# Kernel tuning notes

Measured on AMD Instinct MI355X. Metric: run time of the kernel, lower is better.

## Reference

```python
import jax, jax.numpy as jnp
import numpy as np

DIMS = 1024
STATE = 2 * DIMS
EPS = 1e-8


def _rmsnorm(v, scale):
    # norm = ||v||_2 * d^{-1/2}
    d = v.shape[-1]
    n = jnp.sqrt(jnp.sum(v * v, axis=-1, keepdims=True)) * (d ** -0.5)
    return scale * v / (n + EPS)


def setup_inputs() -> dict:
    key = jax.random.key(0)
    ks = jax.random.split(key, 5)
    x = jax.random.normal(ks[0], (4, 2048, DIMS), dtype=jnp.float32)
    ls_scale = jnp.ones((DIMS // 2,), dtype=jnp.float32)
    rs_scale = jnp.ones((DIMS // 2,), dtype=jnp.float32)
    split_scale = jnp.full((DIMS,), 0.1, dtype=jnp.float32)
    sk = (1.0 / DIMS) ** 0.5
    Wk = jax.random.uniform(ks[1], (DIMS, STATE), jnp.float32, -sk, sk)
    Wugg = jax.random.uniform(ks[2], (DIMS, 3 * STATE), jnp.float32, -sk, sk)
    so = (1.0 / STATE) ** 0.5
    Wout = jax.random.uniform(ks[3], (STATE, DIMS), jnp.float32, -so, so)
    return {"x": x, "ls_scale": ls_scale, "rs_scale": rs_scale,
            "split_scale": split_scale, "Wk": Wk, "Wugg": Wugg, "Wout": Wout}


def reference(x, ls_scale, rs_scale, split_scale, Wk, Wugg, Wout):
    residual = x
    # RMS_split norm (output_dim=None)
    xl, xr = jnp.split(x, 2, axis=-1)
    xn = jnp.concatenate([_rmsnorm(xl, ls_scale), _rmsnorm(xr, rs_scale)], axis=-1)
    xn = xn * split_scale

    K = jax.nn.sigmoid(xn @ Wk)                      # [B,S,STATE]
    u, g_in, g_out = jnp.split(xn @ Wugg, 3, axis=-1)
    u = u * jax.nn.sigmoid(g_in) * (1.0 - K)

    # linear recurrence: h_0 = u_0; h_t = K_{t-1} * h_{t-1} + u_t
    a = jnp.concatenate([jnp.ones_like(K[..., :1, :]), K[..., :-1, :]], axis=-2)

    def combine(lhs, rhs):
        aL, bL = lhs
        aR, bR = rhs
        return (aL * aR, bL * aR + bR)

    _, h = jax.lax.associative_scan(combine, (a, u), axis=1)
    outputs = h * jax.nn.sigmoid(g_out)
    y = outputs @ Wout
    return y + residual
```

## Files before the change

kernel.cpp:

```cpp
#include <hip/hip_runtime.h>
#include <hip/hip_bf16.h>
#include <hip/hip_fp8.h>
#include <stdint.h>

#define DIMS 1024
#define STATE 2048
#define BATCH 4
#define SEQ 2048
#define TOKENS 8192
#define N1 8192
#define NCHUNK 16
#define CHUNKL (SEQ / NCHUNK)

typedef __hip_bfloat16 bf16;
typedef unsigned char u8;
typedef unsigned short u16;
typedef __attribute__((ext_vector_type(4))) float f32x4;
typedef __attribute__((ext_vector_type(16))) float f32x16;
typedef __attribute__((ext_vector_type(2))) long v2i64;

#define XN_SCALE 32.0f
#define W1_SCALE 256.0f
#define H_SCALE  32.0f
#define W2_SCALE 256.0f
#define INV_SCALE (1.0f / 8192.0f)

__device__ __forceinline__ float sigmoidf_(float x) {
  return 1.0f / (1.0f + __expf(-x));
}

__device__ __forceinline__ u8 to_fp8(float f) {
  __hip_fp8_e4m3 h(f);
  return h.__x;
}

__device__ __forceinline__ float b2f(u16 v) {
  union { uint32_t u; float f; } w;
  w.u = ((uint32_t)v) << 16;
  return w.f;
}

__device__ __forceinline__ u16 f2b(float f) {
  bf16 h = __float2bfloat16(f);
  return *(u16*)&h;
}

__device__ __forceinline__ int kperm(int k) {
  return (k & ~24) | ((k & 8) << 1) | ((k & 16) >> 1);
}

__device__ __forceinline__ void async_copy16(const void* g, void* l) {
  __builtin_amdgcn_global_load_lds(
      (const __attribute__((address_space(1))) void*)(uintptr_t)g,
      (__attribute__((address_space(3))) void*)(uint32_t)(uintptr_t)l,
      16, 0, 0);
}

__device__ __forceinline__ int swz32(int row, int kc) {
  int line = row >> 1;
  int sub = ((row & 1) << 2) | kc;
  return (line << 3) | (sub ^ (line & 7));
}
__device__ __forceinline__ void swz32_dec(int c, int& row, int& kc) {
  int line = c >> 3;
  int sub = (c & 7) ^ (line & 7);
  row = (line << 1) | (sub >> 2);
  kc = sub & 3;
}

__device__ __forceinline__ int xcd_swz(int wg, int nwg) {
  return (wg & 7) * (nwg >> 3) + (wg >> 3);
}

__global__ __launch_bounds__(256) void transpose_fp8_kernel(
    const float* __restrict__ W, u8* __restrict__ Wt, int K, int N,
    int stream_base, int interleave, float scale) {
  __shared__ float tile[32][33];
  int tx = threadIdx.x & 31;
  int ty = threadIdx.x >> 5;
  long col = (long)blockIdx.x * 32 + tx;
  long rowb = (long)blockIdx.y * 32;
#pragma unroll
  for (int i = 0; i < 32; i += 8)
    tile[ty + i][tx] = W[(rowb + ty + i) * N + col];
  __syncthreads();
  long ocol = rowb + kperm(tx);
  long orow = (long)blockIdx.x * 32 + ty;
#pragma unroll
  for (int i = 0; i < 32; i += 8) {
    long n = orow + i;
    long dstrow = interleave ? (((n & 2047) << 2) | (stream_base + (n >> 11))) : n;
    Wt[dstrow * K + ocol] = to_fp8(tile[tx][ty + i] * scale);
  }
}

__global__ __launch_bounds__(256) void rmsnorm_kernel(
    const float* __restrict__ x, const float* __restrict__ ls,
    const float* __restrict__ rs, const float* __restrict__ ss,
    u8* __restrict__ xn8) {
  int token = blockIdx.x;
  int tid = threadIdx.x;
  const float4* xt = (const float4*)(x + (long)token * DIMS);
  float4 v = xt[tid];
  float s = v.x * v.x + v.y * v.y + v.z * v.z + v.w * v.w;
#pragma unroll
  for (int d = 32; d > 0; d >>= 1) s += __shfl_down(s, d);
  __shared__ float parts[4];
  if ((tid & 63) == 0) parts[tid >> 6] = s;
  __syncthreads();
  int j = tid * 4;
  bool left = j < 512;
  float sum = left ? (parts[0] + parts[1]) : (parts[2] + parts[3]);
  float n = sqrtf(sum * (1.0f / 512.0f));
  float inv = 1.0f / (n + 1e-8f);
  const float4* sc = (const float4*)(left ? ls : rs);
  float4 g = sc[left ? tid : tid - 128];
  float4 p = ((const float4*)ss)[tid];
  u8 q[4];
  q[0] = to_fp8(v.x * g.x * inv * p.x * XN_SCALE);
  q[1] = to_fp8(v.y * g.y * inv * p.y * XN_SCALE);
  q[2] = to_fp8(v.z * g.z * inv * p.z * XN_SCALE);
  q[3] = to_fp8(v.w * g.w * inv * p.w * XN_SCALE);
  *(uint32_t*)(xn8 + (long)token * DIMS + kperm(j)) = *(uint32_t*)q;
}

__device__ __forceinline__ void g1f8_stage(const u8* __restrict__ A,
                                           const u8* __restrict__ Bt,
                                           long arow0, long brow0, int k0,
                                           int wave, int lane, u8* As, u8* Bs) {
  const int K = DIMS;
#pragma unroll
  for (int i = 0; i < 4; i++) {
    int c = (wave * 4 + i) * 64 + lane;
    int row, kc; swz32_dec(c, row, kc);
    async_copy16(A + (arow0 + row) * K + k0 + kc * 16, (char*)As + (wave * 4 + i) * 1024);
  }
#pragma unroll
  for (int i = 0; i < 2; i++) {
    int c = (wave * 2 + i) * 64 + lane;
    int row, kc; swz32_dec(c, row, kc);
    async_copy16(Bt + (brow0 + row) * K + k0 + kc * 16, (char*)Bs + (wave * 2 + i) * 1024);
  }
}

__global__ __launch_bounds__(256, 2) void gemm1_fp8(
    const u8* __restrict__ A, const u8* __restrict__ Bt,
    uint32_t* __restrict__ AU, u16* __restrict__ GO) {
  __shared__ __align__(16) u8 As[3][256 * 64];
  __shared__ __align__(16) u8 Bs[3][128 * 64];
  int tid = threadIdx.x;
  int lane = tid & 63, wave = tid >> 6;
  int wm = wave & 1, wn = wave >> 1;
  int wg = xcd_swz(blockIdx.y * gridDim.x + blockIdx.x, gridDim.x * gridDim.y);
  int bx = wg & (gridDim.x - 1);
  int by = wg >> 6;
  long arow0 = (long)by * 256;
  long brow0 = (long)bx * 128;
  int m_lane = lane & 31, q4 = lane >> 5;
  f32x16 acc[4][2] = {};

  g1f8_stage(A, Bt, arow0, brow0, 0, wave, lane, As[0], Bs[0]);
  g1f8_stage(A, Bt, arow0, brow0, 64, wave, lane, As[1], Bs[1]);

  int cur = 0, nxt = 2;
  for (int it = 0; it < 16; ++it) {
    if (it == 15) asm volatile("s_waitcnt vmcnt(0)" ::: "memory");
    else          asm volatile("s_waitcnt vmcnt(6)" ::: "memory");
    __builtin_amdgcn_s_barrier();
    __builtin_amdgcn_sched_barrier(0);
    if (it + 2 < 16)
      g1f8_stage(A, Bt, arow0, brow0, (it + 2) * 64, wave, lane, As[nxt], Bs[nxt]);
    const u8* Asc = As[cur];
    const u8* Bsc = Bs[cur];
    v2i64 af[2][4], bfr[2][2];
#pragma unroll
    for (int p = 0; p < 2; p++) {
#pragma unroll
      for (int mt = 0; mt < 4; mt++)
        af[p][mt] = *(const v2i64*)(Asc + swz32(wm * 128 + mt * 32 + m_lane, p * 2 + q4) * 16);
#pragma unroll
      for (int nt = 0; nt < 2; nt++)
        bfr[p][nt] = *(const v2i64*)(Bsc + swz32(wn * 64 + nt * 32 + m_lane, p * 2 + q4) * 16);
    }
    __builtin_amdgcn_s_setprio(1);
#pragma unroll
    for (int p = 0; p < 2; p++)
#pragma unroll
      for (int mt = 0; mt < 4; mt++)
#pragma unroll
        for (int nt = 0; nt < 2; nt++) {
          acc[mt][nt] = __builtin_amdgcn_mfma_f32_32x32x16_fp8_fp8(bfr[p][nt][0], af[p][mt][0], acc[mt][nt], 0, 0, 0);
          acc[mt][nt] = __builtin_amdgcn_mfma_f32_32x32x16_fp8_fp8(bfr[p][nt][1], af[p][mt][1], acc[mt][nt], 0, 0, 0);
        }
    __builtin_amdgcn_s_setprio(0);
    cur = cur == 2 ? 0 : cur + 1;
    nxt = nxt == 2 ? 0 : nxt + 1;
  }

#pragma unroll
  for (int mt = 0; mt < 4; mt++) {
    long row = arow0 + wm * 128 + mt * 32 + m_lane;
    long rb = row * STATE;
#pragma unroll
    for (int nt = 0; nt < 2; nt++) {
#pragma unroll
      for (int g = 0; g < 4; g++) {
        long col = brow0 + wn * 64 + nt * 32 + g * 8 + q4 * 4;
        long ch = col >> 2;
        float kraw = acc[mt][nt][g * 4 + 0] * INV_SCALE;
        float uraw = acc[mt][nt][g * 4 + 1] * INV_SCALE;
        float gin  = acc[mt][nt][g * 4 + 2] * INV_SCALE;
        float gout = acc[mt][nt][g * 4 + 3] * INV_SCALE;
        float ah = sigmoidf_(kraw);
        float uu = uraw * sigmoidf_(gin) * (1.0f - ah);
        u16 pr[2];
        pr[0] = f2b(ah);
        pr[1] = f2b(uu);
        AU[rb + ch] = *(uint32_t*)pr;
        GO[rb + ch] = f2b(sigmoidf_(gout));
      }
    }
  }
}

__device__ __forceinline__ void g2f8_stage(const u8* __restrict__ A,
                                           const u8* __restrict__ Bt,
                                           long arow0, long brow0, int k0,
                                           int wave, int lane, u8* As, u8* Bs) {
  const int K = STATE;
#pragma unroll
  for (int i = 0; i < 2; i++) {
    int c = (wave * 2 + i) * 64 + lane;
    int row, kc; swz32_dec(c, row, kc);
    async_copy16(A + (arow0 + row) * K + k0 + kc * 16, (char*)As + (wave * 2 + i) * 1024);
  }
#pragma unroll
  for (int i = 0; i < 2; i++) {
    int c = (wave * 2 + i) * 64 + lane;
    int row, kc; swz32_dec(c, row, kc);
    async_copy16(Bt + (brow0 + row) * K + k0 + kc * 16, (char*)Bs + (wave * 2 + i) * 1024);
  }
}

__global__ __launch_bounds__(256) void gemm2_fp8(
    const u8* __restrict__ A, const u8* __restrict__ Bt,
    float* __restrict__ C, const float* __restrict__ resid) {
  __shared__ __align__(16) u8 As[3][128 * 64];
  __shared__ __align__(16) u8 Bs[3][128 * 64];
  int tid = threadIdx.x;
  int lane = tid & 63, wave = tid >> 6;
  int wm = wave & 1, wn = wave >> 1;
  int wg = xcd_swz(blockIdx.y * gridDim.x + blockIdx.x, gridDim.x * gridDim.y);
  int bx = wg & (gridDim.x - 1);
  int by = wg >> 3;
  long arow0 = (long)by * 128;
  long brow0 = (long)bx * 128;
  int m_lane = lane & 31, q4 = lane >> 5;
  f32x16 acc[2][2] = {};

  g2f8_stage(A, Bt, arow0, brow0, 0, wave, lane, As[0], Bs[0]);
  g2f8_stage(A, Bt, arow0, brow0, 64, wave, lane, As[1], Bs[1]);

  int cur = 0, nxt = 2;
  for (int it = 0; it < 32; ++it) {
    if (it == 31) asm volatile("s_waitcnt vmcnt(0)" ::: "memory");
    else          asm volatile("s_waitcnt vmcnt(4)" ::: "memory");
    __builtin_amdgcn_s_barrier();
    __builtin_amdgcn_sched_barrier(0);
    if (it + 2 < 32)
      g2f8_stage(A, Bt, arow0, brow0, (it + 2) * 64, wave, lane, As[nxt], Bs[nxt]);
    const u8* Asc = As[cur];
    const u8* Bsc = Bs[cur];
    v2i64 af[2][2], bfr[2][2];
#pragma unroll
    for (int p = 0; p < 2; p++) {
#pragma unroll
      for (int mt = 0; mt < 2; mt++)
        af[p][mt] = *(const v2i64*)(Asc + swz32(wm * 64 + mt * 32 + m_lane, p * 2 + q4) * 16);
#pragma unroll
      for (int nt = 0; nt < 2; nt++)
        bfr[p][nt] = *(const v2i64*)(Bsc + swz32(wn * 64 + nt * 32 + m_lane, p * 2 + q4) * 16);
    }
    __builtin_amdgcn_s_setprio(1);
#pragma unroll
    for (int p = 0; p < 2; p++)
#pragma unroll
      for (int mt = 0; mt < 2; mt++)
#pragma unroll
        for (int nt = 0; nt < 2; nt++) {
          acc[mt][nt] = __builtin_amdgcn_mfma_f32_32x32x16_fp8_fp8(bfr[p][nt][0], af[p][mt][0], acc[mt][nt], 0, 0, 0);
          acc[mt][nt] = __builtin_amdgcn_mfma_f32_32x32x16_fp8_fp8(bfr[p][nt][1], af[p][mt][1], acc[mt][nt], 0, 0, 0);
        }
    __builtin_amdgcn_s_setprio(0);
    cur = cur == 2 ? 0 : cur + 1;
    nxt = nxt == 2 ? 0 : nxt + 1;
  }
#pragma unroll
  for (int mt = 0; mt < 2; mt++) {
    long row = arow0 + wm * 64 + mt * 32 + m_lane;
#pragma unroll
    for (int nt = 0; nt < 2; nt++) {
#pragma unroll
      for (int g = 0; g < 4; g++) {
        long col = brow0 + wn * 64 + nt * 32 + g * 8 + q4 * 4;
        float4 rv = *(const float4*)(resid + row * DIMS + col);
        float4 ov;
        ov.x = acc[mt][nt][g * 4 + 0] * INV_SCALE + rv.x;
        ov.y = acc[mt][nt][g * 4 + 1] * INV_SCALE + rv.y;
        ov.z = acc[mt][nt][g * 4 + 2] * INV_SCALE + rv.z;
        ov.w = acc[mt][nt][g * 4 + 3] * INV_SCALE + rv.w;
        *(float4*)(C + row * DIMS + col) = ov;
      }
    }
  }
}

__global__ __launch_bounds__(256) void chunk_summary_kernel(
    const uint32_t* __restrict__ AU, float* __restrict__ carryA,
    float* __restrict__ carryU) {
  int b = blockIdx.x;
  int ch = blockIdx.y * 256 + threadIdx.x;
  int chunk = blockIdx.z;
  int t0 = chunk * CHUNKL;
  const uint32_t* base = AU + (long)b * SEQ * STATE + ch;
  float ap = 1.0f;
  if (chunk != 0) ap = b2f((u16)(base[(long)(t0 - 1) * STATE] & 0xffff));
  float A = 1.0f, U = 0.0f;
#pragma unroll 8
  for (int t = t0; t < t0 + CHUNKL; t++) {
    uint32_t w = base[(long)t * STATE];
    float ah = b2f((u16)(w & 0xffff));
    float u  = b2f((u16)(w >> 16));
    A *= ap;
    U = ap * U + u;
    ap = ah;
  }
  int cidx = (b * NCHUNK + chunk) * STATE + ch;
  carryA[cidx] = A;
  carryU[cidx] = U;
}

__global__ __launch_bounds__(256) void carry_scan_kernel(
    const float* __restrict__ carryA, const float* __restrict__ carryU,
    float* __restrict__ carryIn) {
  int idx = blockIdx.x * 256 + threadIdx.x;
  int b = idx >> 11;
  int ch = idx & 2047;
  float h = 0.0f;
#pragma unroll
  for (int c = 0; c < NCHUNK; c++) {
    int cidx = (b * NCHUNK + c) * STATE + ch;
    carryIn[cidx] = h;
    h = carryA[cidx] * h + carryU[cidx];
  }
}

__global__ __launch_bounds__(256) void scan_chunk_kernel(
    const uint32_t* __restrict__ AU, const u16* __restrict__ GO,
    const float* __restrict__ carryIn, u8* __restrict__ sco8) {
  int b = blockIdx.x;
  int c0 = blockIdx.y * 32;
  int chunk = blockIdx.z;
  int tstart = chunk * CHUNKL;
  __shared__ float a_s[32][65], u_s[32][65], h_s[32][65];
  int tid = threadIdx.x;
  int lane = tid & 63, wave = tid >> 6;
  int cc = tid & 31;
  int tq = tid >> 5;

  float carryH[8], carryK[8];
#pragma unroll
  for (int i = 0; i < 8; i++) {
    int ch = c0 + wave * 8 + i;
    carryH[i] = carryIn[(b * NCHUNK + chunk) * STATE + ch];
    carryK[i] = (chunk == 0)
                    ? 1.0f
                    : b2f((u16)(AU[((long)(b * SEQ + tstart - 1)) * STATE + ch] & 0xffff));
  }

  float g_r[8];
  for (int t0 = tstart; t0 < tstart + CHUNKL; t0 += 64) {
#pragma unroll
    for (int i = 0; i < 8; i++) {
      int t = tq * 8 + i;
      long idx = ((long)(b * SEQ + t0 + t)) * STATE + c0 + cc;
      uint32_t w = AU[idx];
      a_s[cc][t] = b2f((u16)(w & 0xffff));
      u_s[cc][t] = b2f((u16)(w >> 16));
      g_r[i] = b2f(GO[idx]);
    }
    __syncthreads();
#pragma unroll
    for (int i = 0; i < 8; i++) {
      int ch = wave * 8 + i;
      float aK = a_s[ch][lane];
      float u = u_s[ch][lane];
      float a = __shfl_up(aK, 1);
      if (lane == 0) a = carryK[i];
      float A = a, U = u;
#pragma unroll
      for (int d = 1; d < 64; d <<= 1) {
        float Au = __shfl_up(A, d);
        float Uu = __shfl_up(U, d);
        if (lane >= d) { U += A * Uu; A *= Au; }
      }
      float h = U + A * carryH[i];
      carryH[i] = __shfl(h, 63);
      carryK[i] = __shfl(aK, 63);
      h_s[ch][lane] = h;
    }
    __syncthreads();
#pragma unroll
    for (int i = 0; i < 8; i++) {
      int t = tq * 8 + i;
      sco8[((long)(b * SEQ + t0 + t)) * STATE + c0 + kperm(cc)] =
          to_fp8(h_s[cc][t] * g_r[i] * H_SCALE);
    }
    __syncthreads();
  }
}

extern "C" void kernel_launch(void* const* d_in, const int* in_sizes, int n_in,
                              void* d_out, int out_size, void* d_ws, size_t ws_size,
                              hipStream_t stream) {
  const float* x    = (const float*)d_in[0];
  const float* ls   = (const float*)d_in[1];
  const float* rs   = (const float*)d_in[2];
  const float* ss   = (const float*)d_in[3];
  const float* Wk   = (const float*)d_in[4];
  const float* Wugg = (const float*)d_in[5];
  const float* Wout = (const float*)d_in[6];
  float* out = (float*)d_out;

  char* ws = (char*)d_ws;
  u8*   W1f8 = (u8*)ws;
  u8*   W2f8 = (u8*)(ws + 8388608);
  u8*   xn8  = (u8*)(ws + 10485760);
  uint32_t* AU = (uint32_t*)(ws + 18874368);
  u16*  GOb  = (u16*)(ws + 18874368 + 67108864);
  u8*   sco8 = (u8*)(ws + 18874368 + 67108864 + 33554432);
  float* carryA  = (float*)xn8;
  float* carryU  = carryA + BATCH * NCHUNK * STATE;
  float* carryIn = carryU + BATCH * NCHUNK * STATE;

  transpose_fp8_kernel<<<dim3(STATE / 32, DIMS / 32), 256, 0, stream>>>(
      Wk, W1f8, DIMS, STATE, 0, 1, W1_SCALE);
  transpose_fp8_kernel<<<dim3(3 * STATE / 32, DIMS / 32), 256, 0, stream>>>(
      Wugg, W1f8, DIMS, 3 * STATE, 1, 1, W1_SCALE);
  transpose_fp8_kernel<<<dim3(DIMS / 32, STATE / 32), 256, 0, stream>>>(
      Wout, W2f8, STATE, DIMS, 0, 0, W2_SCALE);

  rmsnorm_kernel<<<TOKENS, 256, 0, stream>>>(x, ls, rs, ss, xn8);

  gemm1_fp8<<<dim3(N1 / 128, TOKENS / 256), 256, 0, stream>>>(xn8, W1f8, AU, GOb);

  chunk_summary_kernel<<<dim3(BATCH, STATE / 256, NCHUNK), 256, 0, stream>>>(
      AU, carryA, carryU);
  carry_scan_kernel<<<dim3(BATCH * STATE / 256), 256, 0, stream>>>(
      carryA, carryU, carryIn);
  scan_chunk_kernel<<<dim3(BATCH, STATE / 32, NCHUNK), 256, 0, stream>>>(
      AU, GOb, carryIn, sco8);

  gemm2_fp8<<<dim3(DIMS / 128, TOKENS / 128), 256, 0, stream>>>(
      sco8, W2f8, out, x);
}
```

Baseline: 399.6 us.

## Enlarge gemm1 tile to 256x256 with 8 waves and phased load/MFMA interleave

The first FP8 GEMM now uses 256x256 output tiles computed by 512 threads (8 waves, 2x4) instead of 256x128 tiles with 4 waves. Each K step is split into four phases, and each phase issues one slice of the next stage's async global-to-LDS copies alongside a small batch of MFMAs, separated by barriers. The aim is better operand reuse per byte loaded and finer overlap of memory traffic with matrix math. In exchange, LDS use rises to about 96KB per block, which likely limits the CU to one resident block, and each K step now has many more barriers.

```diff
diff --git a/kernel.cpp b/kernel.cpp
--- a/kernel.cpp
+++ b/kernel.cpp
@@ -124,77 +124,124 @@
   *(uint32_t*)(xn8 + (long)token * DIMS + kperm(j)) = *(uint32_t*)q;
 }
 
-__device__ __forceinline__ void g1f8_stage(const u8* __restrict__ A,
-                                           const u8* __restrict__ Bt,
-                                           long arow0, long brow0, int k0,
-                                           int wave, int lane, u8* As, u8* Bs) {
-  const int K = DIMS;
-#pragma unroll
-  for (int i = 0; i < 4; i++) {
-    int c = (wave * 4 + i) * 64 + lane;
+__device__ __forceinline__ void g1_stage_q(
+    const u8* __restrict__ A, const u8* __restrict__ Bt,
+    long arow0, long brow0, int k0, int q, int wave, int lane,
+    u8* As, u8* Bs) {
+  int cb = q * 512 + wave * 64;
+  int c = cb + lane;
+  if (cb < 1024) {
     int row, kc; swz32_dec(c, row, kc);
-    async_copy16(A + (arow0 + row) * K + k0 + kc * 16, (char*)As + (wave * 4 + i) * 1024);
-  }
-#pragma unroll
-  for (int i = 0; i < 2; i++) {
-    int c = (wave * 2 + i) * 64 + lane;
-    int row, kc; swz32_dec(c, row, kc);
-    async_copy16(Bt + (brow0 + row) * K + k0 + kc * 16, (char*)Bs + (wave * 2 + i) * 1024);
-  }
-}
-
-__global__ __launch_bounds__(256, 2) void gemm1_fp8(
+    async_copy16(A + (arow0 + row) * DIMS + k0 + kc * 16, As + cb * 16);
+  } else {
+    int row, kc; swz32_dec(c - 1024, row, kc);
+    async_copy16(Bt + (brow0 + row) * DIMS + k0 + kc * 16, Bs + (cb - 1024) * 16);
+  }
+}
+
+__global__ __launch_bounds__(512, 2) void gemm1_fp8(
     const u8* __restrict__ A, const u8* __restrict__ Bt,
     uint32_t* __restrict__ AU, u16* __restrict__ GO) {
   __shared__ __align__(16) u8 As[3][256 * 64];
-  __shared__ __align__(16) u8 Bs[3][128 * 64];
+  __shared__ __align__(16) u8 Bs[3][256 * 64];
   int tid = threadIdx.x;
-  int lane = tid & 63, wave = tid >> 6;
-  int wm = wave & 1, wn = wave >> 1;
+  int lane = tid & 63;
+  int wave = tid >> 6;
+  int wm = wave >> 2;
+  int wn = wave & 3;
   int wg = xcd_swz(blockIdx.y * gridDim.x + blockIdx.x, gridDim.x * gridDim.y);
-  int bx = wg & (gridDim.x - 1);
-  int by = wg >> 6;
+  int bx = wg & 31;
+  int by = wg >> 5;
   long arow0 = (long)by * 256;
-  long brow0 = (long)bx * 128;
+  long brow0 = (long)bx * 256;
   int m_lane = lane & 31, q4 = lane >> 5;
   f32x16 acc[4][2] = {};
 
-  g1f8_stage(A, Bt, arow0, brow0, 0, wave, lane, As[0], Bs[0]);
-  g1f8_stage(A, Bt, arow0, brow0, 64, wave, lane, As[1], Bs[1]);
-
-  int cur = 0, nxt = 2;
-  for (int it = 0; it < 16; ++it) {
-    if (it == 15) asm volatile("s_waitcnt vmcnt(0)" ::: "memory");
-    else          asm volatile("s_waitcnt vmcnt(6)" ::: "memory");
-    __builtin_amdgcn_s_barrier();
+#pragma unroll
+  for (int q = 0; q < 4; q++)
+    g1_stage_q(A, Bt, arow0, brow0, 0, q, wave, lane, As[0], Bs[0]);
+#pragma unroll
+  for (int q = 0; q < 4; q++)
+    g1_stage_q(A, Bt, arow0, brow0, 64, q, wave, lane, As[1], Bs[1]);
+  asm volatile("s_waitcnt vmcnt(4)" ::: "memory");
+  __builtin_amdgcn_s_barrier();
+
+  int bufc = 0, bufn = 2;
+  for (int t = 0; t < 16; ++t) {
+    const u8* Asc = As[bufc];
+    const u8* Bsc = Bs[bufc];
+    u8* Asn = As[bufn];
+    u8* Bsn = Bs[bufn];
+    int k2 = (t + 2) * 64;
+    bool pf = (t + 2 < 16);
+    v2i64 af[4], bfr;
+
+#pragma unroll
+    for (int mt = 0; mt < 4; mt++)
+      af[mt] = *(const v2i64*)(Asc + swz32(wm * 128 + mt * 32 + m_lane, q4) * 16);
+    bfr = *(const v2i64*)(Bsc + swz32(wn * 64 + m_lane, q4) * 16);
+    if (pf) g1_stage_q(A, Bt, arow0, brow0, k2, 0, wave, lane, Asn, Bsn);
+    __builtin_amdgcn_s_barrier();
+    asm volatile("s_waitcnt lgkmcnt(0)" ::: "memory");
     __builtin_amdgcn_sched_barrier(0);
-    if (it + 2 < 16)
-      g1f8_stage(A, Bt, arow0, brow0, (it + 2) * 64, wave, lane, As[nxt], Bs[nxt]);
-    const u8* Asc = As[cur];
-    const u8* Bsc = Bs[cur];
-    v2i64 af[2][4], bfr[2][2];
-#pragma unroll
-    for (int p = 0; p < 2; p++) {
-#pragma unroll
-      for (int mt = 0; mt < 4; mt++)
-        af[p][mt] = *(const v2i64*)(Asc + swz32(wm * 128 + mt * 32 + m_lane, p * 2 + q4) * 16);
-#pragma unroll
-      for (int nt = 0; nt < 2; nt++)
-        bfr[p][nt] = *(const v2i64*)(Bsc + swz32(wn * 64 + nt * 32 + m_lane, p * 2 + q4) * 16);
-    }
     __builtin_amdgcn_s_setprio(1);
 #pragma unroll
-    for (int p = 0; p < 2; p++)
-#pragma unroll
-      for (int mt = 0; mt < 4; mt++)
-#pragma unroll
-        for (int nt = 0; nt < 2; nt++) {
-          acc[mt][nt] = __builtin_amdgcn_mfma_f32_32x32x16_fp8_fp8(bfr[p][nt][0], af[p][mt][0], acc[mt][nt], 0, 0, 0);
-          acc[mt][nt] = __builtin_amdgcn_mfma_f32_32x32x16_fp8_fp8(bfr[p][nt][1], af[p][mt][1], acc[mt][nt], 0, 0, 0);
-        }
+    for (int mt = 0; mt < 4; mt++) {
+      acc[mt][0] = __builtin_amdgcn_mfma_f32_32x32x16_fp8_fp8(bfr[0], af[mt][0], acc[mt][0], 0, 0, 0);
+      acc[mt][0] = __builtin_amdgcn_mfma_f32_32x32x16_fp8_fp8(bfr[1], af[mt][1], acc[mt][0], 0, 0, 0);
+    }
     __builtin_amdgcn_s_setprio(0);
-    cur = cur == 2 ? 0 : cur + 1;
-    nxt = nxt == 2 ? 0 : nxt + 1;
+    __builtin_amdgcn_s_barrier();
+
+    bfr = *(const v2i64*)(Bsc + swz32(wn * 64 + 32 + m_lane, q4) * 16);
+    if (pf) g1_stage_q(A, Bt, arow0, brow0, k2, 1, wave, lane, Asn, Bsn);
+    __builtin_amdgcn_s_barrier();
+    asm volatile("s_waitcnt lgkmcnt(0)" ::: "memory");
+    __builtin_amdgcn_sched_barrier(0);
+    __builtin_amdgcn_s_setprio(1);
+#pragma unroll
+    for (int mt = 0; mt < 4; mt++) {
+      acc[mt][1] = __builtin_amdgcn_mfma_f32_32x32x16_fp8_fp8(bfr[0], af[mt][0], acc[mt][1], 0, 0, 0);
+      acc[mt][1] = __builtin_amdgcn_mfma_f32_32x32x16_fp8_fp8(bfr[1], af[mt][1], acc[mt][1], 0, 0, 0);
+    }
+    __builtin_amdgcn_s_setprio(0);
+    __builtin_amdgcn_s_barrier();
+
+#pragma unroll
+    for (int mt = 0; mt < 4; mt++)
+      af[mt] = *(const v2i64*)(Asc + swz32(wm * 128 + mt * 32 + m_lane, 2 + q4) * 16);
+    bfr = *(const v2i64*)(Bsc + swz32(wn * 64 + m_lane, 2 + q4) * 16);
+    if (pf) g1_stage_q(A, Bt, arow0, brow0, k2, 2, wave, lane, Asn, Bsn);
+    __builtin_amdgcn_s_barrier();
+    asm volatile("s_waitcnt lgkmcnt(0)" ::: "memory");
+    __builtin_amdgcn_sched_barrier(0);
+    __builtin_amdgcn_s_setprio(1);
+#pragma unroll
+    for (int mt = 0; mt < 4; mt++) {
+      acc[mt][0] = __builtin_amdgcn_mfma_f32_32x32x16_fp8_fp8(bfr[0], af[mt][0], acc[mt][0], 0, 0, 0);
+      acc[mt][0] = __builtin_amdgcn_mfma_f32_32x32x16_fp8_fp8(bfr[1], af[mt][1], acc[mt][0], 0, 0, 0);
+    }
+    __builtin_amdgcn_s_setprio(0);
+    __builtin_amdgcn_s_barrier();
+
+    bfr = *(const v2i64*)(Bsc + swz32(wn * 64 + 32 + m_lane, 2 + q4) * 16);
+    if (pf) g1_stage_q(A, Bt, arow0, brow0, k2, 3, wave, lane, Asn, Bsn);
+    if (pf) asm volatile("s_waitcnt vmcnt(4)" ::: "memory");
+    else    asm volatile("s_waitcnt vmcnt(0)" ::: "memory");
+    __builtin_amdgcn_s_barrier();
+    asm volatile("s_waitcnt lgkmcnt(0)" ::: "memory");
+    __builtin_amdgcn_sched_barrier(0);
+    __builtin_amdgcn_s_setprio(1);
+#pragma unroll
+    for (int mt = 0; mt < 4; mt++) {
+      acc[mt][1] = __builtin_amdgcn_mfma_f32_32x32x16_fp8_fp8(bfr[0], af[mt][0], acc[mt][1], 0, 0, 0);
+      acc[mt][1] = __builtin_amdgcn_mfma_f32_32x32x16_fp8_fp8(bfr[1], af[mt][1], acc[mt][1], 0, 0, 0);
+    }
+    __builtin_amdgcn_s_setprio(0);
+    __builtin_amdgcn_s_barrier();
+
+    bufc = bufc == 2 ? 0 : bufc + 1;
+    bufn = bufn == 2 ? 0 : bufn + 1;
   }
 
 #pragma unroll
@@ -452,7 +499,7 @@
 
   rmsnorm_kernel<<<TOKENS, 256, 0, stream>>>(x, ls, rs, ss, xn8);
 
-  gemm1_fp8<<<dim3(N1 / 128, TOKENS / 256), 256, 0, stream>>>(xn8, W1f8, AU, GOb);
+  gemm1_fp8<<<dim3(N1 / 256, TOKENS / 256), 512, 0, stream>>>(xn8, W1f8, AU, GOb);
 
   chunk_summary_kernel<<<dim3(BATCH, STATE / 256, NCHUNK), 256, 0, stream>>>(
       AU, carryA, carryU);
```

Measured after the change: 416.4 us. +4.2%, slower.
